# Kernel tuning notes

Hardware: AMD Instinct MI355X
Metric: run time of the kernel (lower is better)

## Reference

```python
import jax, jax.numpy as jnp
import numpy as np
import math

N, D, F, G = 8192, 512, 2048, 102
GAMMA = 0.5
NEG = -1e9


def setup_inputs() -> dict:
    key = jax.random.key(0)
    ks = jax.random.split(key, 32)
    x = jax.random.normal(ks[0], (N, D), dtype=jnp.float32)
    real_edge_mask = jax.random.bernoulli(ks[1], 0.9, (N, N))  # True = masked (non-edge)
    fake_edge_mask = jax.random.bernoulli(ks[2], 0.1, (N, N))
    # per-row distinct sorted drop indices over gene_list = arange(D)
    r = jax.random.uniform(ks[3], (N, D))
    drop_idx = jnp.sort(jnp.argsort(r, axis=1)[:, :G], axis=1).astype(jnp.int32)
    s = 1.0 / math.sqrt(D)
    def W(k, m, n):
        return jax.random.normal(k, (m, n), dtype=jnp.float32) * s
    inp = {
        'x': x, 'drop_idx': drop_idx,
        'real_edge_mask': real_edge_mask, 'fake_edge_mask': fake_edge_mask,
        'enc_Wq_r': W(ks[4], D, D), 'enc_Wk_r': W(ks[5], D, D),
        'enc_Wq_f': W(ks[6], D, D), 'enc_Wk_f': W(ks[7], D, D), 'enc_Wv': W(ks[8], D, D),
        'dec_Wq_r': W(ks[9], D, D), 'dec_Wk_r': W(ks[10], D, D),
        'dec_Wq_f': W(ks[11], D, D), 'dec_Wk_f': W(ks[12], D, D), 'dec_Wv': W(ks[13], D, D),
        'ff_W1': W(ks[14], D, F), 'ff_b1': jnp.zeros((F,), jnp.float32),
        'ff_W2': W(ks[15], F, D), 'ff_b2': jnp.zeros((D,), jnp.float32),
        'ln1_g': jnp.ones((D,), jnp.float32), 'ln1_b': jnp.zeros((D,), jnp.float32),
        'ln2_g': jnp.ones((D,), jnp.float32), 'ln2_b': jnp.zeros((D,), jnp.float32),
        'ln3_g': jnp.ones((D,), jnp.float32), 'ln3_b': jnp.zeros((D,), jnp.float32),
        'head_W': W(ks[16], D, D), 'head_b': jnp.zeros((D,), jnp.float32),
    }
    return inp


def layer_norm(h, g, b, eps=1e-5):
    mu = h.mean(-1, keepdims=True)
    var = ((h - mu) ** 2).mean(-1, keepdims=True)
    return (h - mu) * jax.lax.rsqrt(var + eps) * g + b


def spatial_attention(h, Wq_r, Wk_r, Wq_f, Wk_f, Wv, rmask, fmask, gamma):
    d = h.shape[-1]
    scale = 1.0 / math.sqrt(d)
    sr = jnp.where(rmask, NEG, (h @ Wq_r) @ (h @ Wk_r).T * scale)  # [N,N]
    sf = jnp.where(fmask, NEG, (h @ Wq_f) @ (h @ Wk_f).T * scale)  # [N,N]
    m = jnp.maximum(sr.max(axis=1, keepdims=True), sf.max(axis=1, keepdims=True))
    scores = (jnp.exp(sr - m) + gamma * jnp.exp(sf - m)) / (1.0 + gamma)
    attn = scores / scores.sum(axis=-1, keepdims=True)
    return attn @ (h @ Wv), attn


def reference(x, drop_idx, real_edge_mask, fake_edge_mask,
              enc_Wq_r, enc_Wk_r, enc_Wq_f, enc_Wk_f, enc_Wv,
              dec_Wq_r, dec_Wk_r, dec_Wq_f, dec_Wk_f, dec_Wv,
              ff_W1, ff_b1, ff_W2, ff_b2,
              ln1_g, ln1_b, ln2_g, ln2_b, ln3_g, ln3_b,
              head_W, head_b):
    rows = jnp.arange(x.shape[0])[:, None]
    drop_x = x.at[rows, drop_idx].set(0.0)
    hidden, _ = spatial_attention(drop_x, enc_Wq_r, enc_Wk_r, enc_Wq_f, enc_Wk_f, enc_Wv,
                                  real_edge_mask, fake_edge_mask, GAMMA)
    hidden = layer_norm(hidden + drop_x, ln1_g, ln1_b)
    ff = jax.nn.gelu(hidden @ ff_W1 + ff_b1, approximate=False) @ ff_W2 + ff_b2
    hidden = layer_norm(hidden + ff, ln2_g, ln2_b)
    recon, _ = spatial_attention(hidden, dec_Wq_r, dec_Wk_r, dec_Wq_f, dec_Wk_f, dec_Wv,
                                 real_edge_mask, fake_edge_mask, GAMMA)
    recon = layer_norm(recon + hidden, ln3_g, ln3_b)
    h = recon @ head_W + head_b
    x_init = jnp.take_along_axis(x, drop_idx, axis=1)    # [N,G]
    x_recon = jnp.take_along_axis(h, drop_idx, axis=1)   # [N,G]
    return x_init, x_recon
```

## Files before the change

kernel.cpp:

```cpp
#include <hip/hip_runtime.h>
#include <cstdint>
#include <cstddef>


typedef unsigned short u16;
typedef __bf16 bf16x8 __attribute__((ext_vector_type(8)));
typedef float f32x4 __attribute__((ext_vector_type(4)));

#define GAMMA_C 0.5f
#define SCALE_C 0.04419417382415922f
#define NG      (8192 * 102)

__device__ __forceinline__ float b2f(u16 u) {
  union { unsigned int i; float f; } c; c.i = ((unsigned int)u) << 16; return c.f;
}
__device__ __forceinline__ u16 f2b(float f) {
  union { float f; unsigned int i; } c; c.f = f;
  unsigned int u = c.i + 0x7FFFu + ((c.i >> 16) & 1u);
  return (u16)(u >> 16);
}
__device__ __forceinline__ float gelu_exact(float x) {
  return 0.5f * x * (1.0f + erff(x * 0.70710678118654752f));
}
__device__ __forceinline__ int idx_at(const void* p, int i, int i64) {
  return i64 ? (int)((const long long*)p)[i] : ((const int*)p)[i];
}
__device__ __forceinline__ float fl_at(const void* p, size_t i, int f32m) {
  return f32m ? ((const float*)p)[i] : b2f(((const u16*)p)[i]);
}
__device__ __forceinline__ void mask8(const void* m, size_t base, int f, bool o[8]) {
  if (f == 1) {
    unsigned long long v = *(const unsigned long long*)((const unsigned char*)m + base);
#pragma unroll
    for (int e = 0; e < 8; ++e) o[e] = ((v >> (8 * e)) & 0xFF) != 0;
  } else if (f == 0) {
    const uint4 a = *(const uint4*)((const int*)m + base);
    const uint4 b = *(const uint4*)((const int*)m + base + 4);
    o[0] = a.x; o[1] = a.y; o[2] = a.z; o[3] = a.w;
    o[4] = b.x; o[5] = b.y; o[6] = b.z; o[7] = b.w;
  } else if (f == 2) {
    const uint4 v = *(const uint4*)((const u16*)m + base);
    const u16* p = (const u16*)&v;
#pragma unroll
    for (int e = 0; e < 8; ++e) o[e] = p[e] != 0;
  } else {
    const uint4 a = *(const uint4*)((const float*)m + base);
    const uint4 b = *(const uint4*)((const float*)m + base + 4);
    o[0] = a.x; o[1] = a.y; o[2] = a.z; o[3] = a.w;
    o[4] = b.x; o[5] = b.y; o[6] = b.z; o[7] = b.w;
  }
}

#define GLD16(g, l) __builtin_amdgcn_global_load_lds(                         \
    (const __attribute__((address_space(1))) void*)(g),                       \
    (__attribute__((address_space(3))) void*)(l), 16, 0, 0)

__global__ void detect_all(const unsigned char* __restrict__ rmask,
                           const void* __restrict__ xin,
                           const void* __restrict__ idx,
                           int* __restrict__ flags) {
  __shared__ int nz[4];
  __shared__ int mx, bl;
  const int t = threadIdx.x;
  if (t < 4) nz[t] = 0;
  if (t == 0) { mx = 0; bl = 0; }
  __syncthreads();
  int cnt = 0, lm = 0;
  for (int i = t; i < 4096; i += 256) {
    const int v = rmask[i];
    if (v) { ++cnt; if (v > lm) lm = v; }
  }
  if (cnt) atomicAdd(&nz[t & 3], cnt);
  if (lm) atomicMax(&mx, lm);
  int bcnt = 0;
  for (int i = t; i < 2048; i += 256) {
    const u16 u = ((const u16*)xin)[2 * i];
    const int e = (u >> 7) & 0xFF;
    if ((e >= 110 && e <= 141) || u == 0) ++bcnt;
  }
  atomicAdd(&bl, bcnt);
  __syncthreads();
  if (t == 0) {
    int f;
    if (nz[1] == 0 && nz[2] == 0 && nz[3] == 0) f = 0;
    else if (nz[0] == 0 && nz[1] == 0) f = 3;
    else if (mx <= 1) f = 1;
    else f = 2;
    flags[0] = f;
    flags[2] = (bl >= 1536) ? 0 : 1;
    int ok = 1, prev = -1;
    for (int j = 0; j < 102; ++j) {
      const int v = ((const int*)idx)[j];
      if (v <= prev || v < 0 || v >= 512) { ok = 0; break; }
      prev = v;
    }
    flags[1] = ok ? 0 : 1;
  }
}

__global__ void bitmask_prep(const void* __restrict__ mr, const void* __restrict__ mf,
                             unsigned char* __restrict__ bmr, unsigned char* __restrict__ bmf,
                             const int* __restrict__ flags) {
  const int i = blockIdx.x * 256 + threadIdx.x;
  const int f = flags[0];
  bool mk[8];
  mask8(mr, (size_t)i * 8, f, mk);
  unsigned char b = 0;
#pragma unroll
  for (int e = 0; e < 8; ++e) b |= (unsigned char)mk[e] << e;
  bmr[i] = b;
  mask8(mf, (size_t)i * 8, f, mk);
  b = 0;
#pragma unroll
  for (int e = 0; e < 8; ++e) b |= (unsigned char)mk[e] << e;
  bmf[i] = b;
}

struct PtrPack { const void* p[11]; };
__global__ void transpose_cvt_b(PtrPack srcs, u16* __restrict__ out,
                                const int* __restrict__ flags) {
  __shared__ u16 tile[32][33];
  const void* in = srcs.p[blockIdx.z];
  u16* o = out + (size_t)blockIdx.z * 512 * 512;
  const int f32m = flags[2];
  const int c0 = blockIdx.x * 32, r0 = blockIdx.y * 32;
  const int tx = threadIdx.x, ty = threadIdx.y;
  for (int i = ty; i < 32; i += 8) {
    const size_t src = (size_t)(r0 + i) * 512 + (c0 + tx);
    tile[i][tx] = f32m ? f2b(((const float*)in)[src]) : ((const u16*)in)[src];
  }
  __syncthreads();
  for (int i = ty; i < 32; i += 8)
    o[(size_t)(c0 + i) * 512 + (r0 + tx)] = tile[tx][i];
}
__global__ void transpose_cvt(const void* __restrict__ in, u16* __restrict__ out,
                              int R, int C, const int* __restrict__ flags) {
  __shared__ u16 tile[32][33];
  const int f32m = flags[2];
  const int c0 = blockIdx.x * 32, r0 = blockIdx.y * 32;
  const int tx = threadIdx.x, ty = threadIdx.y;
  for (int i = ty; i < 32; i += 8) {
    const size_t src = (size_t)(r0 + i) * C + (c0 + tx);
    tile[i][tx] = f32m ? f2b(((const float*)in)[src]) : ((const u16*)in)[src];
  }
  __syncthreads();
  for (int i = ty; i < 32; i += 8)
    out[(size_t)(c0 + i) * R + (r0 + tx)] = tile[tx][i];
}

__global__ void cvt_to_bf16(const void* __restrict__ in, u16* __restrict__ out,
                            int n, const int* __restrict__ flags) {
  const int i = blockIdx.x * blockDim.x + threadIdx.x;
  if (i < n)
    out[i] = flags[2] ? f2b(((const float*)in)[i]) : ((const u16*)in)[i];
}
__global__ void zero_f32(float* __restrict__ p, int n) {
  const int i = blockIdx.x * blockDim.x + threadIdx.x;
  if (i < n) p[i] = 0.f;
}
__global__ void zero_drop(u16* __restrict__ dx, const void* __restrict__ idx,
                          const int* __restrict__ flags) {
  const int i = blockIdx.x * blockDim.x + threadIdx.x;
  if (i < NG) {
    const int row = i / 102;
    dx[(size_t)row * 512 + idx_at(idx, i, flags[1])] = 0;
  }
}
__global__ void gather_out_k(const void* __restrict__ x, const u16* __restrict__ h,
                             const void* __restrict__ idx, void* __restrict__ out,
                             const int* __restrict__ flags) {
  const int i = blockIdx.x * blockDim.x + threadIdx.x;
  if (i < NG) {
    const int row = i / 102;
    const int c = idx_at(idx, i, flags[1]);
    const size_t src = (size_t)row * 512 + c;
    if (flags[2]) {
      ((float*)out)[i] = ((const float*)x)[src];
      ((float*)out)[NG + i] = b2f(h[src]);
    } else {
      ((u16*)out)[i] = ((const u16*)x)[src];
      ((u16*)out)[NG + i] = h[src];
    }
  }
}

__global__ __launch_bounds__(256)
void gemm_bt(const u16* __restrict__ A, int lda,
             const u16* __restrict__ Bt, int ldb,
             u16* __restrict__ C, int ldc,
             int K, int mode, const void* __restrict__ bias,
             const int* __restrict__ flags, u16* __restrict__ aux) {
  __shared__ alignas(16) u16 smem[16384];
  u16* As = smem;
  u16* Bs = smem + 8192;
  const int tid = threadIdx.x;
  const int lane = tid & 63, wave = tid >> 6;
  const int l15 = lane & 15, l4 = lane >> 4;
  const int wm = (wave >> 1) << 6, wn = (wave & 1) << 6;
  const int m0 = blockIdx.y << 7, n0 = blockIdx.x << 7;

  f32x4 acc[4][4];
#pragma unroll
  for (int i = 0; i < 4; ++i)
#pragma unroll
    for (int j = 0; j < 4; ++j) acc[i][j] = (f32x4){0.f, 0.f, 0.f, 0.f};

  const int lrow = lane >> 3;
  const int lcg = (lane & 7) ^ lrow;
  const u16* aG = A + (size_t)(m0 + wave * 8 + lrow) * lda + lcg * 8;
  const u16* bG = Bt + (size_t)(n0 + wave * 8 + lrow) * ldb + lcg * 8;
  u16* asDst = &As[(wave * 8) * 64];
  u16* bsDst = &Bs[(wave * 8) * 64];
  const int swz = (l15 & 7) << 3;

  for (int k0 = 0; k0 < K; k0 += 64) {
#pragma unroll
    for (int r = 0; r < 4; ++r) {
      GLD16(aG + (size_t)(r * 32) * lda + k0, asDst + r * 32 * 64);
      GLD16(bG + (size_t)(r * 32) * ldb + k0, bsDst + r * 32 * 64);
    }
    __syncthreads();
#pragma unroll
    for (int kk = 0; kk < 2; ++kk) {
      bf16x8 a[4], b[4];
      const int koff = (((kk << 2) + l4) << 3) ^ swz;
#pragma unroll
      for (int i = 0; i < 4; ++i) {
        a[i] = *(const bf16x8*)&As[(wm + (i << 4) + l15) * 64 + koff];
        b[i] = *(const bf16x8*)&Bs[(wn + (i << 4) + l15) * 64 + koff];
      }
#pragma unroll
      for (int i = 0; i < 4; ++i)
#pragma unroll
        for (int j = 0; j < 4; ++j)
          acc[i][j] = __builtin_amdgcn_mfma_f32_16x16x32_bf16(a[i], b[j], acc[i][j], 0, 0, 0);
    }
    __syncthreads();
  }

  const int f32m = flags[2];

  if (mode == 2 && n0 >= 2048) {
#pragma unroll
    for (int i = 0; i < 4; ++i) {
      const int rbase = m0 + wm + (i << 4) + l4 * 4;
#pragma unroll
      for (int j = 0; j < 4; ++j) {
        const int gn = n0 - 2048 + wn + (j << 4) + l15;
        ushort4 pk;
        pk.x = f2b(acc[i][j][0]); pk.y = f2b(acc[i][j][1]);
        pk.z = f2b(acc[i][j][2]); pk.w = f2b(acc[i][j][3]);
        *(ushort4*)&aux[(size_t)gn * 8192 + rbase] = pk;
      }
    }
    return;
  }

#pragma unroll
  for (int i = 0; i < 4; ++i) {
    const int rl0 = wm + (i << 4) + l4 * 4;
#pragma unroll
    for (int j = 0; j < 4; ++j) {
      const int cl = wn + (j << 4) + l15;
      float bv = 0.f;
      if (bias) bv = fl_at(bias, n0 + cl, f32m);
      const int chunk = cl >> 3, within = cl & 7;
#pragma unroll
      for (int r = 0; r < 4; ++r) {
        const int rl = rl0 + r;
        float v = acc[i][j][r] + bv;
        if (mode == 1) v = gelu_exact(v);
        const int wchunk = (chunk & 8) | ((chunk ^ rl) & 7);
        smem[rl * 128 + wchunk * 8 + within] = f2b(v);
      }
    }
  }
  __syncthreads();

  const int r = tid >> 1, h = tid & 1;
  const int grow = m0 + r;
#pragma unroll
  for (int cb = 0; cb < 8; ++cb) {
    const int chunkidx = h * 8 + cb;
    const int rchunk = (chunkidx & 8) | ((chunkidx ^ r) & 7);
    uint4 raw = *(const uint4*)&smem[r * 128 + rchunk * 8];
    *(uint4*)&C[(size_t)grow * ldc + n0 + chunkidx * 8] = raw;
  }
}

__global__ __launch_bounds__(256, 3)
void score_fused(const u16* __restrict__ P,
                 const unsigned char* __restrict__ bmr,
                 const unsigned char* __restrict__ bmf,
                 u16* __restrict__ W, float* __restrict__ lvec) {
  __shared__ alignas(16) u16 stage[16384];
  __shared__ unsigned long long mrs[256], mfs[256];
  const int tid = threadIdx.x;
  const int lane = tid & 63, wave = tid >> 6;
  const int l15 = lane & 15, l4 = lane >> 4;
  const int wm = (wave >> 1) << 6, wn = (wave & 1) << 6;
  const int m0 = blockIdx.y << 7, n0 = blockIdx.x << 7;

  {
    const int r = tid >> 1, hh = tid & 1;
    const size_t mo = (size_t)(m0 + r) * 1024 + (n0 >> 3) + hh * 8;
    mrs[tid] = *(const unsigned long long*)&bmr[mo];
    mfs[tid] = *(const unsigned long long*)&bmf[mo];
  }

  const int lrow = lane >> 3;
  const int lcg = (lane & 7) ^ lrow;
  const int swz = (l15 & 7) << 3;
  u16* asDst = &stage[(wave * 8) * 64];
  u16* bsDst = &stage[8192 + (wave * 8) * 64];

  unsigned int srp[4][4][2];
  f32x4 acc[4][4];

  for (int p = 0; p < 2; ++p) {
#pragma unroll
    for (int i = 0; i < 4; ++i)
#pragma unroll
      for (int j = 0; j < 4; ++j) acc[i][j] = (f32x4){0.f, 0.f, 0.f, 0.f};

    const u16* aG = P + (p ? 1024 : 0) + (size_t)(m0 + wave * 8 + lrow) * 2048 + lcg * 8;
    const u16* bG = P + (p ? 1536 : 512) + (size_t)(n0 + wave * 8 + lrow) * 2048 + lcg * 8;

    for (int k0 = 0; k0 < 512; k0 += 64) {
#pragma unroll
      for (int r = 0; r < 4; ++r) {
        GLD16(aG + (size_t)(r * 32) * 2048 + k0, asDst + r * 32 * 64);
        GLD16(bG + (size_t)(r * 32) * 2048 + k0, bsDst + r * 32 * 64);
      }
      __syncthreads();
#pragma unroll
      for (int kk = 0; kk < 2; ++kk) {
        bf16x8 a[4], b[4];
        const int koff = (((kk << 2) + l4) << 3) ^ swz;
#pragma unroll
        for (int i = 0; i < 4; ++i) {
          a[i] = *(const bf16x8*)&stage[(wm + (i << 4) + l15) * 64 + koff];
          b[i] = *(const bf16x8*)&stage[8192 + (wn + (i << 4) + l15) * 64 + koff];
        }
#pragma unroll
        for (int i = 0; i < 4; ++i)
#pragma unroll
          for (int j = 0; j < 4; ++j)
            acc[i][j] = __builtin_amdgcn_mfma_f32_16x16x32_bf16(a[i], b[j], acc[i][j], 0, 0, 0);
      }
      __syncthreads();
    }

    if (p == 0) {
#pragma unroll
      for (int i = 0; i < 4; ++i)
#pragma unroll
        for (int j = 0; j < 4; ++j) {
          srp[i][j][0] = (unsigned int)f2b(acc[i][j][0] * SCALE_C)
                       | ((unsigned int)f2b(acc[i][j][1] * SCALE_C) << 16);
          srp[i][j][1] = (unsigned int)f2b(acc[i][j][2] * SCALE_C)
                       | ((unsigned int)f2b(acc[i][j][3] * SCALE_C) << 16);
        }
    }
  }

  const int hb = wn >> 6;
#pragma unroll
  for (int i = 0; i < 4; ++i) {
    const int rl0 = wm + (i << 4) + l4 * 4;
#pragma unroll
    for (int r = 0; r < 4; ++r) {
      const int rl = rl0 + r;
      const unsigned long long mr = mrs[rl * 2 + hb];
      const unsigned long long mf = mfs[rl * 2 + hb];
      float rsum = 0.f;
#pragma unroll
      for (int j = 0; j < 4; ++j) {
        const int cl = wn + (j << 4) + l15;
        const int bit = cl & 63;
        const float srv = b2f((u16)(srp[i][j][r >> 1] >> ((r & 1) * 16)));
        const float sfv = acc[i][j][r] * SCALE_C;
        const float wr = ((mr >> bit) & 1) ? 0.f : __expf(srv);
        const float wf = ((mf >> bit) & 1) ? 0.f : __expf(sfv);
        const float w = wr + GAMMA_C * wf;
        rsum += w;
        const int chunk = cl >> 3, within = cl & 7;
        const int wchunk = (chunk & 8) | ((chunk ^ rl) & 7);
        stage[rl * 128 + wchunk * 8 + within] = f2b(w);
      }
      rsum += __shfl_xor(rsum, 1);
      rsum += __shfl_xor(rsum, 2);
      rsum += __shfl_xor(rsum, 4);
      rsum += __shfl_xor(rsum, 8);
      if (l15 == 0) atomicAdd(&lvec[m0 + rl], rsum);
    }
  }
  __syncthreads();

  const int rr = tid >> 1, hh = tid & 1;
  const int grow = m0 + rr;
#pragma unroll
  for (int cb = 0; cb < 8; ++cb) {
    const int chunkidx = hh * 8 + cb;
    const int rchunk = (chunkidx & 8) | ((chunkidx ^ rr) & 7);
    uint4 raw = *(const uint4*)&stage[rr * 128 + rchunk * 8];
    *(uint4*)&W[(size_t)grow * 8192 + n0 + chunkidx * 8] = raw;
  }
}

__global__ __launch_bounds__(256)
void gemm_pv_splitk(const u16* __restrict__ W, const u16* __restrict__ Vt,
                    float* __restrict__ Oacc) {
  __shared__ alignas(16) u16 smem[16384];
  u16* As = smem;
  u16* Bs = smem + 8192;
  const int tid = threadIdx.x;
  const int lane = tid & 63, wave = tid >> 6;
  const int l15 = lane & 15, l4 = lane >> 4;
  const int wm = (wave >> 1) << 6, wn = (wave & 1) << 6;
  const int m0 = blockIdx.y << 7, n0 = blockIdx.x << 7;
  const int kbase = blockIdx.z << 11;
  float* Oslab = Oacc + (size_t)blockIdx.z * (8192 * 512);

  f32x4 acc[4][4];
#pragma unroll
  for (int i = 0; i < 4; ++i)
#pragma unroll
    for (int j = 0; j < 4; ++j) acc[i][j] = (f32x4){0.f, 0.f, 0.f, 0.f};

  const int lrow = lane >> 3;
  const int lcg = (lane & 7) ^ lrow;
  const u16* aG = W + (size_t)(m0 + wave * 8 + lrow) * 8192 + lcg * 8 + kbase;
  const u16* bG = Vt + (size_t)(n0 + wave * 8 + lrow) * 8192 + lcg * 8 + kbase;
  u16* asDst = &As[(wave * 8) * 64];
  u16* bsDst = &Bs[(wave * 8) * 64];
  const int swz = (l15 & 7) << 3;

  for (int k0 = 0; k0 < 2048; k0 += 64) {
#pragma unroll
    for (int r = 0; r < 4; ++r) {
      GLD16(aG + (size_t)(r * 32) * 8192 + k0, asDst + r * 32 * 64);
      GLD16(bG + (size_t)(r * 32) * 8192 + k0, bsDst + r * 32 * 64);
    }
    __syncthreads();
#pragma unroll
    for (int kk = 0; kk < 2; ++kk) {
      bf16x8 a[4], b[4];
      const int koff = (((kk << 2) + l4) << 3) ^ swz;
#pragma unroll
      for (int i = 0; i < 4; ++i) {
        a[i] = *(const bf16x8*)&As[(wm + (i << 4) + l15) * 64 + koff];
        b[i] = *(const bf16x8*)&Bs[(wn + (i << 4) + l15) * 64 + koff];
      }
#pragma unroll
      for (int i = 0; i < 4; ++i)
#pragma unroll
        for (int j = 0; j < 4; ++j)
          acc[i][j] = __builtin_amdgcn_mfma_f32_16x16x32_bf16(a[i], b[j], acc[i][j], 0, 0, 0);
    }
    __syncthreads();
  }

#pragma unroll
  for (int i = 0; i < 4; ++i) {
    const int rbase = m0 + wm + (i << 4) + l4 * 4;
#pragma unroll
    for (int j = 0; j < 4; ++j) {
      const int gn = n0 + wn + (j << 4) + l15;
#pragma unroll
      for (int r = 0; r < 4; ++r)
        Oslab[(size_t)(rbase + r) * 512 + gn] = acc[i][j][r];
    }
  }
}

__global__ __launch_bounds__(256)
void pv_ln(const float* __restrict__ Oacc, const float* __restrict__ lvec,
           const u16* __restrict__ res, const void* __restrict__ g,
           const void* __restrict__ be, u16* __restrict__ out,
           const int* __restrict__ flags) {
  const int row = blockIdx.x, tid = threadIdx.x;
  const int f32m = flags[2];
  const size_t off = (size_t)row * 512 + tid * 2;
  const size_t S = (size_t)8192 * 512;
  const float linv = 1.0f / lvec[row];
  const float o0 = Oacc[off] + Oacc[off + S] + Oacc[off + 2 * S] + Oacc[off + 3 * S];
  const float o1 = Oacc[off + 1] + Oacc[off + 1 + S] + Oacc[off + 1 + 2 * S] + Oacc[off + 1 + 3 * S];
  const float v0 = o0 * linv + b2f(res[off]);
  const float v1 = o1 * linv + b2f(res[off + 1]);
  __shared__ float r1[256], r2[256];
  r1[tid] = v0 + v1;
  r2[tid] = v0 * v0 + v1 * v1;
  __syncthreads();
  for (int s = 128; s > 0; s >>= 1) {
    if (tid < s) { r1[tid] += r1[tid + s]; r2[tid] += r2[tid + s]; }
    __syncthreads();
  }
  const float mu = r1[0] * (1.f / 512.f);
  const float var = r2[0] * (1.f / 512.f) - mu * mu;
  const float rs = rsqrtf(var + 1e-5f);
  out[off]     = f2b((v0 - mu) * rs * fl_at(g, tid * 2, f32m)     + fl_at(be, tid * 2, f32m));
  out[off + 1] = f2b((v1 - mu) * rs * fl_at(g, tid * 2 + 1, f32m) + fl_at(be, tid * 2 + 1, f32m));
}

__global__ __launch_bounds__(256)
void ln_fused(const u16* __restrict__ a, const u16* __restrict__ b,
              const void* __restrict__ g, const void* __restrict__ be,
              u16* __restrict__ out, const int* __restrict__ flags) {
  const int row = blockIdx.x, tid = threadIdx.x;
  const int f32m = flags[2];
  const size_t off = (size_t)row * 512 + tid * 2;
  const float v0 = b2f(a[off]) + b2f(b[off]);
  const float v1 = b2f(a[off + 1]) + b2f(b[off + 1]);
  __shared__ float r1[256], r2[256];
  r1[tid] = v0 + v1;
  r2[tid] = v0 * v0 + v1 * v1;
  __syncthreads();
  for (int s = 128; s > 0; s >>= 1) {
    if (tid < s) { r1[tid] += r1[tid + s]; r2[tid] += r2[tid + s]; }
    __syncthreads();
  }
  const float mu = r1[0] * (1.f / 512.f);
  const float var = r2[0] * (1.f / 512.f) - mu * mu;
  const float rs = rsqrtf(var + 1e-5f);
  out[off]     = f2b((v0 - mu) * rs * fl_at(g, tid * 2, f32m)     + fl_at(be, tid * 2, f32m));
  out[off + 1] = f2b((v1 - mu) * rs * fl_at(g, tid * 2 + 1, f32m) + fl_at(be, tid * 2 + 1, f32m));
}

extern "C" void kernel_launch(void* const* d_in, const int* in_sizes, int n_in,
                              void* d_out, int out_size, void* d_ws, size_t ws_size,
                              hipStream_t stream) {
  (void)in_sizes; (void)n_in; (void)out_size; (void)ws_size;
  const void* x = d_in[0];
  const void* dropidx = d_in[1];
  const void* rmask = d_in[2];
  const void* fmask = d_in[3];

  char* base = (char*)d_ws;
  size_t cur = 0;
  auto alloc = [&](size_t b) -> void* {
    void* p = base + cur;
    cur += (b + 255) & ~(size_t)255;
    return p;
  };

  int* flags = (int*)alloc(256);
  u16* Wt = (u16*)alloc((size_t)11 * 512 * 512 * 2);
  u16* wff1t = (u16*)alloc((size_t)2048 * 512 * 2);
  u16* wff2t = (u16*)alloc((size_t)512 * 2048 * 2);
  const size_t ND2 = (size_t)8192 * 512 * 2;
  u16* dropx = (u16*)alloc(ND2);
  u16* P = (u16*)alloc((size_t)8192 * 2048 * 2);
  u16* Vt = (u16*)alloc(ND2);
  u16* H1 = (u16*)alloc(ND2);
  u16* H2 = (u16*)alloc(ND2);
  u16* FF2 = (u16*)alloc(ND2);
  u16* FF1 = (u16*)alloc((size_t)8192 * 2048 * 2);
  unsigned char* bmr = (unsigned char*)alloc((size_t)8192 * 1024);
  unsigned char* bmf = (unsigned char*)alloc((size_t)8192 * 1024);
  float* lvec = (float*)alloc((size_t)8192 * 4);
  float* Oacc = (float*)alloc((size_t)4 * 8192 * 512 * 4);
  u16* Wb = (u16*)alloc((size_t)8192 * 8192 * 2);

  detect_all<<<1, 256, 0, stream>>>((const unsigned char*)rmask, x, dropidx, flags);
  bitmask_prep<<<32768, 256, 0, stream>>>(rmask, fmask, bmr, bmf, flags);

  const dim3 tb(32, 8);
  PtrPack wp;
  for (int i = 0; i < 5; ++i) wp.p[i] = d_in[4 + i];
  for (int i = 0; i < 5; ++i) wp.p[5 + i] = d_in[9 + i];
  wp.p[10] = d_in[24];
  transpose_cvt_b<<<dim3(16, 16, 11), tb, 0, stream>>>(wp, Wt, flags);
  transpose_cvt<<<dim3(64, 16), tb, 0, stream>>>(d_in[14], wff1t, 512, 2048, flags);
  transpose_cvt<<<dim3(16, 64), tb, 0, stream>>>(d_in[16], wff2t, 2048, 512, flags);

  cvt_to_bf16<<<(8192 * 512 + 255) / 256, 256, 0, stream>>>(x, dropx, 8192 * 512, flags);
  zero_drop<<<(NG + 255) / 256, 256, 0, stream>>>(dropx, dropidx, flags);

  auto gemm = [&](const u16* A, int lda, const u16* Bt, int ldb, u16* Cc, int ldc,
                  int M, int Nn, int K, int mode, const void* bias, u16* aux) {
    gemm_bt<<<dim3(Nn / 128, M / 128), 256, 0, stream>>>(
        A, lda, Bt, ldb, Cc, ldc, K, mode, bias, flags, aux);
  };

  auto attention = [&](const u16* Hin, const u16* Wqkv, const void* lnG,
                       const void* lnB, u16* outLN) {
    zero_f32<<<32, 256, 0, stream>>>(lvec, 8192);
    gemm(Hin, 512, Wqkv, 512, P, 2048, 8192, 2560, 512, 2, nullptr, Vt);
    score_fused<<<dim3(64, 64), 256, 0, stream>>>(P, bmr, bmf, Wb, lvec);
    gemm_pv_splitk<<<dim3(4, 64, 4), 256, 0, stream>>>(Wb, Vt, Oacc);
    pv_ln<<<8192, 256, 0, stream>>>(Oacc, lvec, Hin, lnG, lnB, outLN, flags);
  };

  attention(dropx, Wt, d_in[18], d_in[19], H1);
  gemm(H1, 512, wff1t, 512, FF1, 2048, 8192, 2048, 512, 1, d_in[15], nullptr);
  gemm(FF1, 2048, wff2t, 2048, FF2, 512, 8192, 512, 2048, 0, d_in[17], nullptr);
  ln_fused<<<8192, 256, 0, stream>>>(H1, FF2, d_in[20], d_in[21], H2, flags);
  attention(H2, Wt + (size_t)5 * 512 * 512, d_in[22], d_in[23], H1);
  gemm(H1, 512, Wt + (size_t)10 * 512 * 512, 512, FF2, 512, 8192, 512, 512, 0,
       d_in[25], nullptr);
  gather_out_k<<<(NG + 255) / 256, 256, 0, stream>>>(x, FF2, dropidx, d_out, flags);
}
```

Measured before the change: 1.547 ms.

## Unify split-K GEMMs into gemm_bt with bf16 slabs reduced in LayerNorm kernels

Adds a split-K dimension (blockIdx.z) to the generic gemm_bt and uses it for the PV product (8-way, bf16 slabs instead of 4-way fp32), the FF2 GEMM (2-way) and the head GEMM (2-way). The partial slabs are summed, with bias and residual, inside pv_ln, a new ff_ln and gather_out_k, which also folds the bias add into those consumers. This aims to raise occupancy and parallelism for the narrow N=512 GEMMs and to cut partial-sum traffic by storing partials in bf16. Launch bounds are also raised to 4 waves per SIMD for gemm_bt and score_fused. Storing partials in bf16 adds rounding error, and the extra slabs add reads in the reduction kernels.

Result: slower. 1.602 ms (+3.6%).

```diff
diff --git a/kernel.cpp b/kernel.cpp
--- a/kernel.cpp
+++ b/kernel.cpp
@@ -10,6 +10,7 @@
 #define GAMMA_C 0.5f
 #define SCALE_C 0.04419417382415922f
 #define NG      (8192 * 102)
+#define SLAB    ((size_t)8192 * 512)
 
 __device__ __forceinline__ float b2f(u16 u) {
   union { unsigned int i; float f; } c; c.i = ((unsigned int)u) << 16; return c.f;
@@ -166,7 +167,8 @@
     dx[(size_t)row * 512 + idx_at(idx, i, flags[1])] = 0;
   }
 }
-__global__ void gather_out_k(const void* __restrict__ x, const u16* __restrict__ h,
+__global__ void gather_out_k(const void* __restrict__ x, const u16* __restrict__ hs,
+                             const void* __restrict__ hb,
                              const void* __restrict__ idx, void* __restrict__ out,
                              const int* __restrict__ flags) {
   const int i = blockIdx.x * blockDim.x + threadIdx.x;
@@ -174,22 +176,24 @@
     const int row = i / 102;
     const int c = idx_at(idx, i, flags[1]);
     const size_t src = (size_t)row * 512 + c;
+    const float hv = b2f(hs[src]) + b2f(hs[src + SLAB]) + fl_at(hb, c, flags[2]);
     if (flags[2]) {
       ((float*)out)[i] = ((const float*)x)[src];
-      ((float*)out)[NG + i] = b2f(h[src]);
+      ((float*)out)[NG + i] = hv;
     } else {
       ((u16*)out)[i] = ((const u16*)x)[src];
-      ((u16*)out)[NG + i] = h[src];
-    }
-  }
-}
-
-__global__ __launch_bounds__(256)
+      ((u16*)out)[NG + i] = f2b(hv);
+    }
+  }
+}
+
+__global__ __launch_bounds__(256, 4)
 void gemm_bt(const u16* __restrict__ A, int lda,
              const u16* __restrict__ Bt, int ldb,
              u16* __restrict__ C, int ldc,
              int K, int mode, const void* __restrict__ bias,
-             const int* __restrict__ flags, u16* __restrict__ aux) {
+             const int* __restrict__ flags, u16* __restrict__ aux,
+             long long slabStride) {
   __shared__ alignas(16) u16 smem[16384];
   u16* As = smem;
   u16* Bs = smem + 8192;
@@ -198,6 +202,8 @@
   const int l15 = lane & 15, l4 = lane >> 4;
   const int wm = (wave >> 1) << 6, wn = (wave & 1) << 6;
   const int m0 = blockIdx.y << 7, n0 = blockIdx.x << 7;
+  const size_t kShift = (size_t)blockIdx.z * (size_t)K;
+  C += (size_t)blockIdx.z * (size_t)slabStride;
 
   f32x4 acc[4][4];
 #pragma unroll
@@ -207,8 +213,8 @@
 
   const int lrow = lane >> 3;
   const int lcg = (lane & 7) ^ lrow;
-  const u16* aG = A + (size_t)(m0 + wave * 8 + lrow) * lda + lcg * 8;
-  const u16* bG = Bt + (size_t)(n0 + wave * 8 + lrow) * ldb + lcg * 8;
+  const u16* aG = A + kShift + (size_t)(m0 + wave * 8 + lrow) * lda + lcg * 8;
+  const u16* bG = Bt + kShift + (size_t)(n0 + wave * 8 + lrow) * ldb + lcg * 8;
   u16* asDst = &As[(wave * 8) * 64];
   u16* bsDst = &Bs[(wave * 8) * 64];
   const int swz = (l15 & 7) << 3;
@@ -288,7 +294,7 @@
   }
 }
 
-__global__ __launch_bounds__(256, 3)
+__global__ __launch_bounds__(256, 4)
 void score_fused(const u16* __restrict__ P,
                  const unsigned char* __restrict__ bmr,
                  const unsigned char* __restrict__ bmf,
@@ -409,83 +415,20 @@
 }
 
 __global__ __launch_bounds__(256)
-void gemm_pv_splitk(const u16* __restrict__ W, const u16* __restrict__ Vt,
-                    float* __restrict__ Oacc) {
-  __shared__ alignas(16) u16 smem[16384];
-  u16* As = smem;
-  u16* Bs = smem + 8192;
-  const int tid = threadIdx.x;
-  const int lane = tid & 63, wave = tid >> 6;
-  const int l15 = lane & 15, l4 = lane >> 4;
-  const int wm = (wave >> 1) << 6, wn = (wave & 1) << 6;
-  const int m0 = blockIdx.y << 7, n0 = blockIdx.x << 7;
-  const int kbase = blockIdx.z << 11;
-  float* Oslab = Oacc + (size_t)blockIdx.z * (8192 * 512);
-
-  f32x4 acc[4][4];
-#pragma unroll
-  for (int i = 0; i < 4; ++i)
-#pragma unroll
-    for (int j = 0; j < 4; ++j) acc[i][j] = (f32x4){0.f, 0.f, 0.f, 0.f};
-
-  const int lrow = lane >> 3;
-  const int lcg = (lane & 7) ^ lrow;
-  const u16* aG = W + (size_t)(m0 + wave * 8 + lrow) * 8192 + lcg * 8 + kbase;
-  const u16* bG = Vt + (size_t)(n0 + wave * 8 + lrow) * 8192 + lcg * 8 + kbase;
-  u16* asDst = &As[(wave * 8) * 64];
-  u16* bsDst = &Bs[(wave * 8) * 64];
-  const int swz = (l15 & 7) << 3;
-
-  for (int k0 = 0; k0 < 2048; k0 += 64) {
-#pragma unroll
-    for (int r = 0; r < 4; ++r) {
-      GLD16(aG + (size_t)(r * 32) * 8192 + k0, asDst + r * 32 * 64);
-      GLD16(bG + (size_t)(r * 32) * 8192 + k0, bsDst + r * 32 * 64);
-    }
-    __syncthreads();
-#pragma unroll
-    for (int kk = 0; kk < 2; ++kk) {
-      bf16x8 a[4], b[4];
-      const int koff = (((kk << 2) + l4) << 3) ^ swz;
-#pragma unroll
-      for (int i = 0; i < 4; ++i) {
-        a[i] = *(const bf16x8*)&As[(wm + (i << 4) + l15) * 64 + koff];
-        b[i] = *(const bf16x8*)&Bs[(wn + (i << 4) + l15) * 64 + koff];
-      }
-#pragma unroll
-      for (int i = 0; i < 4; ++i)
-#pragma unroll
-        for (int j = 0; j < 4; ++j)
-          acc[i][j] = __builtin_amdgcn_mfma_f32_16x16x32_bf16(a[i], b[j], acc[i][j], 0, 0, 0);
-    }
-    __syncthreads();
-  }
-
-#pragma unroll
-  for (int i = 0; i < 4; ++i) {
-    const int rbase = m0 + wm + (i << 4) + l4 * 4;
-#pragma unroll
-    for (int j = 0; j < 4; ++j) {
-      const int gn = n0 + wn + (j << 4) + l15;
-#pragma unroll
-      for (int r = 0; r < 4; ++r)
-        Oslab[(size_t)(rbase + r) * 512 + gn] = acc[i][j][r];
-    }
-  }
-}
-
-__global__ __launch_bounds__(256)
-void pv_ln(const float* __restrict__ Oacc, const float* __restrict__ lvec,
+void pv_ln(const u16* __restrict__ slabs, const float* __restrict__ lvec,
            const u16* __restrict__ res, const void* __restrict__ g,
            const void* __restrict__ be, u16* __restrict__ out,
            const int* __restrict__ flags) {
   const int row = blockIdx.x, tid = threadIdx.x;
   const int f32m = flags[2];
   const size_t off = (size_t)row * 512 + tid * 2;
-  const size_t S = (size_t)8192 * 512;
   const float linv = 1.0f / lvec[row];
-  const float o0 = Oacc[off] + Oacc[off + S] + Oacc[off + 2 * S] + Oacc[off + 3 * S];
-  const float o1 = Oacc[off + 1] + Oacc[off + 1 + S] + Oacc[off + 1 + 2 * S] + Oacc[off + 1 + 3 * S];
+  float o0 = 0.f, o1 = 0.f;
+#pragma unroll
+  for (int s = 0; s < 8; ++s) {
+    o0 += b2f(slabs[off + s * SLAB]);
+    o1 += b2f(slabs[off + 1 + s * SLAB]);
+  }
   const float v0 = o0 * linv + b2f(res[off]);
   const float v1 = o1 * linv + b2f(res[off + 1]);
   __shared__ float r1[256], r2[256];
@@ -504,14 +447,17 @@
 }
 
 __global__ __launch_bounds__(256)
-void ln_fused(const u16* __restrict__ a, const u16* __restrict__ b,
-              const void* __restrict__ g, const void* __restrict__ be,
-              u16* __restrict__ out, const int* __restrict__ flags) {
+void ff_ln(const u16* __restrict__ slabs, const void* __restrict__ bias,
+           const u16* __restrict__ res, const void* __restrict__ g,
+           const void* __restrict__ be, u16* __restrict__ out,
+           const int* __restrict__ flags) {
   const int row = blockIdx.x, tid = threadIdx.x;
   const int f32m = flags[2];
   const size_t off = (size_t)row * 512 + tid * 2;
-  const float v0 = b2f(a[off]) + b2f(b[off]);
-  const float v1 = b2f(a[off + 1]) + b2f(b[off + 1]);
+  const float v0 = b2f(slabs[off]) + b2f(slabs[off + SLAB])
+                 + fl_at(bias, tid * 2, f32m) + b2f(res[off]);
+  const float v1 = b2f(slabs[off + 1]) + b2f(slabs[off + 1 + SLAB])
+                 + fl_at(bias, tid * 2 + 1, f32m) + b2f(res[off + 1]);
   __shared__ float r1[256], r2[256];
   r1[tid] = v0 + v1;
   r2[tid] = v0 * v0 + v1 * v1;
@@ -554,12 +500,11 @@
   u16* Vt = (u16*)alloc(ND2);
   u16* H1 = (u16*)alloc(ND2);
   u16* H2 = (u16*)alloc(ND2);
-  u16* FF2 = (u16*)alloc(ND2);
   u16* FF1 = (u16*)alloc((size_t)8192 * 2048 * 2);
   unsigned char* bmr = (unsigned char*)alloc((size_t)8192 * 1024);
   unsigned char* bmf = (unsigned char*)alloc((size_t)8192 * 1024);
   float* lvec = (float*)alloc((size_t)8192 * 4);
-  float* Oacc = (float*)alloc((size_t)4 * 8192 * 512 * 4);
+  u16* slabs = (u16*)alloc((size_t)8 * SLAB * 2);
   u16* Wb = (u16*)alloc((size_t)8192 * 8192 * 2);
 
   detect_all<<<1, 256, 0, stream>>>((const unsigned char*)rmask, x, dropidx, flags);
@@ -578,26 +523,30 @@
   zero_drop<<<(NG + 255) / 256, 256, 0, stream>>>(dropx, dropidx, flags);
 
   auto gemm = [&](const u16* A, int lda, const u16* Bt, int ldb, u16* Cc, int ldc,
-                  int M, int Nn, int K, int mode, const void* bias, u16* aux) {
-    gemm_bt<<<dim3(Nn / 128, M / 128), 256, 0, stream>>>(
-        A, lda, Bt, ldb, Cc, ldc, K, mode, bias, flags, aux);
+                  int M, int Nn, int K, int mode, const void* bias, u16* aux,
+                  int zc, long long slabStride) {
+    gemm_bt<<<dim3(Nn / 128, M / 128, zc), 256, 0, stream>>>(
+        A, lda, Bt, ldb, Cc, ldc, K, mode, bias, flags, aux, slabStride);
   };
 
   auto attention = [&](const u16* Hin, const u16* Wqkv, const void* lnG,
                        const void* lnB, u16* outLN) {
     zero_f32<<<32, 256, 0, stream>>>(lvec, 8192);
-    gemm(Hin, 512, Wqkv, 512, P, 2048, 8192, 2560, 512, 2, nullptr, Vt);
+    gemm(Hin, 512, Wqkv, 512, P, 2048, 8192, 2560, 512, 2, nullptr, Vt, 1, 0);
     score_fused<<<dim3(64, 64), 256, 0, stream>>>(P, bmr, bmf, Wb, lvec);
-    gemm_pv_splitk<<<dim3(4, 64, 4), 256, 0, stream>>>(Wb, Vt, Oacc);
-    pv_ln<<<8192, 256, 0, stream>>>(Oacc, lvec, Hin, lnG, lnB, outLN, flags);
+    gemm(Wb, 8192, Vt, 8192, slabs, 512, 8192, 512, 1024, 0, nullptr, nullptr,
+         8, (long long)SLAB);
+    pv_ln<<<8192, 256, 0, stream>>>(slabs, lvec, Hin, lnG, lnB, outLN, flags);
   };
 
   attention(dropx, Wt, d_in[18], d_in[19], H1);
-  gemm(H1, 512, wff1t, 512, FF1, 2048, 8192, 2048, 512, 1, d_in[15], nullptr);
-  gemm(FF1, 2048, wff2t, 2048, FF2, 512, 8192, 512, 2048, 0, d_in[17], nullptr);
-  ln_fused<<<8192, 256, 0, stream>>>(H1, FF2, d_in[20], d_in[21], H2, flags);
+  gemm(H1, 512, wff1t, 512, FF1, 2048, 8192, 2048, 512, 1, d_in[15], nullptr, 1, 0);
+  gemm(FF1, 2048, wff2t, 2048, slabs, 512, 8192, 512, 1024, 0, nullptr, nullptr,
+       2, (long long)SLAB);
+  ff_ln<<<8192, 256, 0, stream>>>(slabs, d_in[17], H1, d_in[20], d_in[21], H2, flags);
   attention(H2, Wt + (size_t)5 * 512 * 512, d_in[22], d_in[23], H1);
-  gemm(H1, 512, Wt + (size_t)10 * 512 * 512, 512, FF2, 512, 8192, 512, 512, 0,
-       d_in[25], nullptr);
-  gather_out_k<<<(NG + 255) / 256, 256, 0, stream>>>(x, FF2, dropidx, d_out, flags);
-}
+  gemm(H1, 512, Wt + (size_t)10 * 512 * 512, 512, slabs, 512, 8192, 512, 256, 0,
+       nullptr, nullptr, 2, (long long)SLAB);
+  gather_out_k<<<(NG + 255) / 256, 256, 0, stream>>>(x, slabs, d_in[25], dropidx,
+                                                     d_out, flags);
+}
```
